# Kernel tuning notes

Measured on AMD Instinct MI355X. Metric: run time of the kernel, lower is better.

The kernel has to match this reference:

```python
import jax, jax.numpy as jnp
import numpy as np


def _gru_dir(x, Wih, Whh, bih, bhh):
    # x: (B,T,I) -> (B,T,H); torch GRU equations, h0 = 0
    H = Whh.shape[1]
    pre = x @ Wih.T + bih  # (B,T,3H), input projection hoisted out of scan
    def step(h, p):
        gh = h @ Whh.T + bhh
        pr, pz, pn = jnp.split(p, 3, axis=-1)
        gr, gz, gn = jnp.split(gh, 3, axis=-1)
        r = jax.nn.sigmoid(pr + gr)
        z = jax.nn.sigmoid(pz + gz)
        n = jnp.tanh(pn + r * gn)
        h = (1.0 - z) * n + z * h
        return h, h
    h0 = jnp.zeros((x.shape[0], H), x.dtype)
    _, ys = jax.lax.scan(step, h0, jnp.swapaxes(pre, 0, 1))
    return jnp.swapaxes(ys, 0, 1)


def _gru_bidir(x, Wih, Whh, bih, bhh):
    f = _gru_dir(x, Wih[0], Whh[0], bih[0], bhh[0])
    b = _gru_dir(x[:, ::-1], Wih[1], Whh[1], bih[1], bhh[1])[:, ::-1]
    return jnp.concatenate([f, b], axis=-1)


def _forward(inputs, embed, l_Wih, l_Whh, l_bih, l_bhh, r_Wih, r_Whh, r_bih, r_bhh,
             a_Wih, a_Whh, a_bih, a_bhh, Wc1, Wc2, vc, Wb, Wd, vd, Wm, vm, Ws, vs,
             Wp, vp, Wpred):
    x = embed[inputs]  # (B,T,E)
    hl = _gru_bidir(x, l_Wih, l_Whh, l_bih, l_bhh)  # (B,T,2H)
    hr = _gru_bidir(x, r_Wih, r_Whh, r_bih, r_bhh)  # (B,T,2H)
    # co-attention: score[b,i,j] = vc . tanh(Wc1 hl_j + Wc2 hr_i)
    s = jnp.tanh((hl @ Wc1.T)[:, None, :, :] + (hr @ Wc2.T)[:, :, None, :])  # (B,T,T,H)
    ptc = jax.nn.softmax((s @ vc.T)[..., 0], axis=-1) @ hl
    # bilinear: hr (Wb hl)^T
    sjt = jnp.einsum('bid,bjd->bij', hr, hl @ Wb.T)
    ptb = jax.nn.softmax(sjt, axis=-1) @ hl
    # multiplicative: vd . tanh(Wd (hl_j * hr_i))
    p = hl[:, None, :, :] * hr[:, :, None, :]  # (B,T,T,2H)
    ptd = jax.nn.softmax((jnp.tanh(p @ Wd.T) @ vd.T)[..., 0], axis=-1) @ hl
    # subtractive: vm . tanh(Wm (hl_j - hr_i))
    d = hl[:, None, :, :] - hr[:, :, None, :]  # (B,T,T,2H)
    ptm = jax.nn.softmax((jnp.tanh(d @ Wm.T) @ vm.T)[..., 0], axis=-1) @ hl
    # self-attention on hr: vs . tanh(Ws (hr_j * hr_i))
    ss = hr[:, None, :, :] * hr[:, :, None, :]  # (B,T,T,2H)
    pts = jax.nn.softmax((jnp.tanh(ss @ Ws.T) @ vs.T)[..., 0], axis=-1) @ hr
    agg = jnp.concatenate([hr, pts, ptc, ptd, ptb, ptm], axis=-1)  # (B,T,12H)
    ar = _gru_bidir(agg, a_Wih, a_Whh, a_bih, a_bhh)  # (B,T,2H)
    # pooling of hl
    sj = jax.nn.softmax(jnp.swapaxes(jnp.tanh(hl @ Wp.T) @ vp.T, 1, 2), axis=-1)  # (B,1,T)
    rl = sj @ hl  # (B,1,2H)
    # final attention over aggregation
    sj2 = jax.nn.softmax(jnp.swapaxes((ar @ Wc1.T + rl @ Wc2.T) @ vc.T, 1, 2), axis=-1)  # (B,1,T)
    rr = (sj2 @ ar)[:, 0, :]  # (B,2H)
    return jax.nn.sigmoid(rr @ Wpred.T)  # (B,labels)


def setup_inputs() -> dict:
    B, T, V, E, H, L = 4, 256, 30000, 300, 128, 2
    key = jax.random.key(0)
    ks = jax.random.split(key, 40)
    inp = {}
    inp['inputs'] = jax.random.randint(ks[0], (B, T), 0, V)
    inp['embed'] = jax.random.uniform(ks[1], (V, E), jnp.float32, -0.1, 0.1)
    ki = 2
    for name, isz in [('l', E), ('r', E), ('a', 12 * H)]:
        inp[name + '_Wih'] = jax.random.normal(ks[ki], (2, 3 * H, isz), jnp.float32) * 0.05; ki += 1
        inp[name + '_Whh'] = jax.random.normal(ks[ki], (2, 3 * H, H), jnp.float32) * 0.05; ki += 1
        inp[name + '_bih'] = jnp.zeros((2, 3 * H), jnp.float32)
        inp[name + '_bhh'] = jnp.zeros((2, 3 * H), jnp.float32)
    for n, o, i in [('Wc1', H, 2 * H), ('Wc2', H, 2 * H), ('vc', 1, H), ('Wb', 2 * H, 2 * H),
                    ('Wd', H, 2 * H), ('vd', 1, H), ('Wm', H, 2 * H), ('vm', 1, H),
                    ('Ws', H, 2 * H), ('vs', 1, H), ('Wp', H, 2 * H), ('vp', 1, H),
                    ('Wpred', L, 2 * H)]:
        inp[n] = jax.random.normal(ks[ki], (o, i), jnp.float32) * 0.05; ki += 1
    return inp


def reference(inputs, embed, l_Wih, l_Whh, l_bih, l_bhh, r_Wih, r_Whh, r_bih, r_bhh,
              a_Wih, a_Whh, a_bih, a_bhh, Wc1, Wc2, vc, Wb, Wd, vd, Wm, vm, Ws, vs,
              Wp, vp, Wpred):
    return _forward(inputs, embed, l_Wih, l_Whh, l_bih, l_bhh, r_Wih, r_Whh, r_bih,
                    r_bhh, a_Wih, a_Whh, a_bih, a_bhh, Wc1, Wc2, vc, Wb, Wd, vd, Wm,
                    vm, Ws, vs, Wp, vp, Wpred)
```

## Files before the change

kernel.cpp:

```cpp
#include <hip/hip_runtime.h>


#define DEV static __device__ __forceinline__
#define BAR_LGKM() __asm__ volatile("s_waitcnt lgkmcnt(0)\ns_barrier" ::: "memory")

typedef __attribute__((ext_vector_type(4))) float f32x4;
typedef __attribute__((ext_vector_type(8))) short s16x8;
typedef __attribute__((ext_vector_type(4))) unsigned int u32x4;
typedef __attribute__((ext_vector_type(2))) unsigned int u32x2;

constexpr int T = 256, E = 300, EP = 320, H = 128, H2 = 256, H3 = 384, H12 = 1536;
constexpr int M = 1024;
constexpr int STY = 262144;

DEV float b2f(unsigned short h) { return __uint_as_float(((unsigned)h) << 16); }
DEV unsigned short f2b(float f) {
  unsigned u = __float_as_uint(f);
  u += 0x7fff + ((u >> 16) & 1);
  return (unsigned short)(u >> 16);
}
DEV unsigned cvt_pk_bf16(float lo, float hi) {
  unsigned r;
  __asm__("v_cvt_pk_bf16_f32 %0, %1, %2" : "=v"(r) : "v"(lo), "v"(hi));
  return r;
}
DEV float rcp_f(float x) {
  float r;
  __asm__("v_rcp_f32 %0, %1" : "=v"(r) : "v"(x));
  return r;
}
DEV float sigm(float x) { return rcp_f(1.f + __expf(-x)); }
DEV float tanh_f(float x) {
  float e = __expf(2.f * x);
  return __builtin_fmaf(-2.f, rcp_f(e + 1.f), 1.f);
}
DEV float plsel(float x0, float x1) {
  u32x2 r = __builtin_amdgcn_permlane32_swap(
      __float_as_uint(x0), __float_as_uint(x1), false, false);
  return __uint_as_float(r[0]);
}

DEV s16x8 ldfrag(const unsigned short* p) {
  u32x4 v = *(const u32x4*)p;
  return __builtin_bit_cast(s16x8, v);
}
DEV f32x4 mfma16(s16x8 a, s16x8 b, f32x4 c) {
  return __builtin_amdgcn_mfma_f32_16x16x32_bf16(a, b, c, 0, 0, 0);
}


struct StageArgs {
  const float* cs[3]; unsigned short* cd[3]; int cn[3];
  const int* idx; const float* emb; unsigned short* xhi; unsigned short* xlo;
  const float* lW; const float* rW; unsigned short* wpad;
  int bo[6];
};

__global__ void k_stage(StageArgs sa) {
  int blk = blockIdx.x;
  int seg = 0;
  #pragma unroll
  for (int s2 = 1; s2 < 5; ++s2) seg = (blk >= sa.bo[s2]) ? s2 : seg;
  int i = (blk - sa.bo[seg]) * 256 + threadIdx.x;
  if (seg < 3) {
    if (i < sa.cn[seg]) sa.cd[seg][i] = f2b(sa.cs[seg][i]);
    return;
  }
  if (seg == 3) {
    if (i >= M * EP) return;
    int m = i / EP, e = i - m * EP;
    int r = sa.idx[m];
    float v = (e < E) ? sa.emb[(size_t)r * E + e] : 0.f;
    unsigned short hi = f2b(v);
    sa.xhi[i] = hi;
    sa.xlo[i] = f2b(v - b2f(hi));
    return;
  }
  if (i >= 4 * H3 * EP) return;
  int e = i % EP, n = (i / EP) % H3, uu = i / (EP * H3);
  const float* src = (uu < 2 ? sa.lW : sa.rW) + (size_t)((uu & 1) * H3 + n) * E;
  sa.wpad[i] = (e < E) ? f2b(src[e]) : (unsigned short)0;
}


struct GemmDesc {
  const unsigned short* Ahi; const unsigned short* Alo; const unsigned short* W;
  const float* bias; float* Cf; int N; int K; int tr;
};
struct GemmBatch { GemmDesc d[8]; };

DEV void gemm_body(const GemmDesc& g, int mb, int nb, int tid) {
  int lane = tid & 63, w = tid >> 6, quad = lane >> 4, l16 = lane & 15;
  int K = g.K;
  const unsigned short* Ahp = g.Ahi + (size_t)(mb + w * 16 + l16) * K + quad * 8;
  const unsigned short* Alp = g.Alo + (size_t)(mb + w * 16 + l16) * K + quad * 8;
  const unsigned short* Wp = g.W + (size_t)(nb + l16) * K + quad * 8;
  f32x4 acc[4];
  #pragma unroll
  for (int nt = 0; nt < 4; ++nt) acc[nt] = f32x4{0.f, 0.f, 0.f, 0.f};
  for (int k = 0; k < K; k += 32) {
    s16x8 ah = ldfrag(Ahp + k);
    s16x8 al = ldfrag(Alp + k);
    #pragma unroll
    for (int nt = 0; nt < 4; ++nt) {
      s16x8 b = ldfrag(Wp + (size_t)nt * 16 * K + k);
      acc[nt] = mfma16(ah, b, acc[nt]);
      acc[nt] = mfma16(al, b, acc[nt]);
    }
  }
  int mr0 = mb + w * 16 + quad * 4;
  #pragma unroll
  for (int nt = 0; nt < 4; ++nt) {
    int col = nb + nt * 16 + l16;
    float bv = g.bias ? g.bias[col] : 0.f;
    #pragma unroll
    for (int r = 0; r < 4; ++r) {
      if (g.tr)
        g.Cf[(size_t)col * M + (mr0 + r)] = acc[nt][r] + bv;
      else
        g.Cf[(size_t)(mr0 + r) * g.N + col] = acc[nt][r] + bv;
    }
  }
}

__global__ __launch_bounds__(256) void k_gemm(GemmBatch gb) {
  GemmDesc g = gb.d[blockIdx.z];
  int nb = blockIdx.y * 64;
  if (nb >= g.N) return;
  gemm_body(g, blockIdx.x * 64, nb, threadIdx.x);
}


struct RecArgs {
  const unsigned short* whh[4];
  const float* pre[4];
  float* outf[4];
  unsigned short* outhi[4];
  unsigned short* outlo[4];
  unsigned short* agghi[4];
  unsigned short* agglo[4];
  const float* bhh[4];
  int colOff[4];
  int dir[4];
  int nGru;
  const float* ccs[6]; unsigned short* ccd[6]; int ccn[6]; int cbo[7];
  const float *Hp, *hlf, *vpf, *Wc2f; float* rlcl;
  const float* Wc1f; const float* vcf; float* uOut;
};

#define GRU_STEP(pr_, pz_, pn_, pq_, hcur_, hnxt_)                             \
  {                                                                            \
    float pr = pr_, pz = pz_, pn = pn_;                                        \
    pq_ += pst2;                                                               \
    pr_ = pq_[0] + bh_r; pz_ = pq_[128] + bh_z; pn_ = pq_[256];                \
    const unsigned short* hb_ = hcur_ + l16 * 136 + quad * 8;                  \
    s16x8 ah0 = ldfrag(hb_);                                                   \
    s16x8 ah1 = ldfrag(hb_ + 32);                                              \
    s16x8 ah2 = ldfrag(hb_ + 64);                                              \
    s16x8 ah3 = ldfrag(hb_ + 96);                                              \
    f32x4 z4 = f32x4{0.f, 0.f, 0.f, 0.f};                                      \
    f32x4 aR0 = mfma16(ah0, bq[0][0], z4);                                     \
    f32x4 aR1 = mfma16(ah2, bq[0][2], z4);                                     \
    aR0 = mfma16(ah1, bq[0][1], aR0);                                          \
    aR1 = mfma16(ah3, bq[0][3], aR1);                                          \
    f32x4 aZ0 = mfma16(ah0, bq[1][0], z4);                                     \
    f32x4 aZ1 = mfma16(ah2, bq[1][2], z4);                                     \
    aZ0 = mfma16(ah1, bq[1][1], aZ0);                                          \
    aZ1 = mfma16(ah3, bq[1][3], aZ1);                                          \
    float r0 = (aR0[0] + aR1[0]) + (aR0[1] + aR1[1]);                          \
    float r1v = (aR0[2] + aR1[2]) + (aR0[3] + aR1[3]);                         \
    float rg = sigm(pr + plsel(r0, r1v));                                      \
    f32x4 aN0 = mfma16(ah0, bq[2][0], z4);                                     \
    f32x4 aN1 = mfma16(ah2, bq[2][2], z4);                                     \
    aN0 = mfma16(ah1, bq[2][1], aN0);                                          \
    aN1 = mfma16(ah3, bq[2][3], aN1);                                          \
    float z0 = (aZ0[0] + aZ1[0]) + (aZ0[1] + aZ1[1]);                          \
    float z1 = (aZ0[2] + aZ1[2]) + (aZ0[3] + aZ1[3]);                          \
    float zg = sigm(pz + plsel(z0, z1));                                       \
    float n0 = (aN0[0] + aN1[0]) + (aN0[1] + aN1[1]);                          \
    float n1 = (aN0[2] + aN1[2]) + (aN0[3] + aN1[3]);                          \
    float ng = tanh_f(pn + rg * (plsel(n0, n1) + bh_n));                       \
    hf = __builtin_fmaf(zg, hf - ng, ng);                                      \
    unsigned hp32 = cvt_pk_bf16(hf, hf);                                       \
    float rem = hf - __uint_as_float(hp32 << 16);                              \
    unsigned lp32 = cvt_pk_bf16(rem, rem);                                     \
    unsigned short hi = (unsigned short)hp32;                                  \
    unsigned short lo = (unsigned short)lp32;                                  \
    hnxt_[(2 * b) * 136 + d] = hi;                                             \
    hnxt_[(2 * b + 1) * 136 + d] = lo;                                         \
    *outf_p = hf; *outhi_p = hi; *outlo_p = lo;                                \
    outf_p += ost; outhi_p += ost; outlo_p += ost;                             \
    if (agghi_p) { *agghi_p = hi; *agglo_p = lo; agghi_p += ast; agglo_p += ast; } \
    BAR_LGKM();                                                                \
  }

__global__ __launch_bounds__(512) void k_gru(RecArgs ra) {
  int blk = blockIdx.x;
  int tid = threadIdx.x;
  if (blk >= ra.nGru) {
    if (ra.rlcl) {
      int b = blk - ra.nGru;
      if (b >= 4) {
        if (tid < 256) {
          float acc = 0.f;
          for (int h = 0; h < 128; ++h)
            acc += ra.vcf[h] * ra.Wc1f[(size_t)h * 256 + tid];
          ra.uOut[tid] = acc;
        }
        return;
      }
      __shared__ float vl[128], wl[256], rvec[256], red[4];
      if (tid < 128) vl[tid] = ra.vpf[tid];
      __syncthreads();
      float s = 0.f, e = 0.f;
      if (tid < 256) {
        const float* hp = ra.Hp + (size_t)(b * 256 + tid) * 128;
        for (int k = 0; k < 128; ++k) s += vl[k] * tanh_f(hp[k]);
        float m = s;
        for (int dl = 32; dl; dl >>= 1) m = fmaxf(m, __shfl_xor(m, dl));
        if ((tid & 63) == 0) red[tid >> 6] = m;
      }
      __syncthreads();
      float m = fmaxf(fmaxf(red[0], red[1]), fmaxf(red[2], red[3]));
      __syncthreads();
      if (tid < 256) {
        e = __expf(s - m);
        float sum = e;
        for (int dl = 32; dl; dl >>= 1) sum += __shfl_xor(sum, dl);
        if ((tid & 63) == 0) red[tid >> 6] = sum;
      }
      __syncthreads();
      float sum = red[0] + red[1] + red[2] + red[3];
      if (tid < 256) wl[tid] = e * rcp_f(sum);
      __syncthreads();
      if (tid < 256) {
        float acc = 0.f;
        for (int t = 0; t < 256; ++t)
          acc += wl[t] * ra.hlf[(size_t)(b * 256 + t) * 256 + tid];
        rvec[tid] = acc;
      }
      __syncthreads();
      if (tid < 128) {
        float a2 = 0.f;
        const float* wr = ra.Wc2f + (size_t)tid * 256;
        for (int dk = 0; dk < 256; ++dk) a2 += rvec[dk] * wr[dk];
        ra.rlcl[b * 128 + tid] = a2;
      }
      return;
    }
    int cb = blk - ra.nGru;
    int seg = 0;
    #pragma unroll
    for (int s2 = 1; s2 < 6; ++s2) seg = (cb >= ra.cbo[s2]) ? s2 : seg;
    int i = (cb - ra.cbo[seg]) * 512 + tid;
    if (i < ra.ccn[seg]) ra.ccd[seg][i] = f2b(ra.ccs[seg][i]);
    return;
  }
  int u = blk;
  __shared__ __align__(16) unsigned short hs[2][16 * 136];
  int lane = tid & 63, w8 = tid >> 6;
  int quad = lane >> 4, l16 = lane & 15;
  for (int i = tid; i < 2 * 16 * 136; i += 512) ((unsigned short*)hs)[i] = 0;
  const unsigned short* whh = ra.whh[u];
  s16x8 bq[3][4];
  #pragma unroll
  for (int g = 0; g < 3; ++g) {
    int row = g * 128 + w8 * 16 + l16;
    #pragma unroll
    for (int kc = 0; kc < 4; ++kc)
      bq[g][kc] = ldfrag(whh + (size_t)row * H + kc * 32 + quad * 8);
  }
  const float* bhh = ra.bhh[u];
  const float* pre = ra.pre[u];
  int colOff = ra.colOff[u], dir = ra.dir[u];
  int b = ((quad & 1) << 1) | (quad >> 1);
  int d = w8 * 16 + l16;
  float bh_r = bhh[d], bh_z = bhh[d + 128], bh_n = bhh[d + 256];
  float hf = 0.f;
  int t0 = dir ? (T - 1) : 0;
  long pst = dir ? -(long)H3 : (long)H3;
  long pst2 = 2 * pst;
  long ost = dir ? -(long)H2 : (long)H2;
  long ast = dir ? -(long)H12 : (long)H12;
  size_t o0 = (size_t)(b * T + t0) * H2 + colOff + d;
  size_t a0 = (size_t)(b * T + t0) * H12 + colOff + d;
  float* outf_p = ra.outf[u] + o0;
  unsigned short* outhi_p = ra.outhi[u] + o0;
  unsigned short* outlo_p = ra.outlo[u] + o0;
  unsigned short* agghi_p = ra.agghi[u] ? ra.agghi[u] + a0 : nullptr;
  unsigned short* agglo_p = ra.agglo[u] ? ra.agglo[u] + a0 : nullptr;
  const float* pqE = pre + (size_t)(b * T + t0) * H3 + d;
  const float* pqO = pqE + pst;
  float e_pr = pqE[0] + bh_r, e_pz = pqE[128] + bh_z, e_pn = pqE[256];
  float o_pr = pqO[0] + bh_r, o_pz = pqO[128] + bh_z, o_pn = pqO[256];
  __syncthreads();
  for (int s = 0; s < T; s += 2) {
    GRU_STEP(e_pr, e_pz, e_pn, pqE, hs[0], hs[1]);
    GRU_STEP(o_pr, o_pz, o_pn, pqO, hs[1], hs[0]);
  }
}


struct ScMMArgs {
  const unsigned short* Xhi[2];
  const float* Rf; const float* Wt[2]; const float* vt[2];
  float* So[2];
};
struct FuseArgs { GemmDesc d[6]; ScMMArgs sm; };

__global__ __launch_bounds__(512, 2) void k_fuse(FuseArgs fa) {
  __shared__ __align__(16) unsigned short w_lds[128 * 256];
  int y = blockIdx.y;
  int tid = threadIdx.x;
  if (y < 6) {
    int xx = blockIdx.x;
    if (xx >= 32) return;
    GemmDesc g = fa.d[y];
    int nb = (xx >> 3) * 64;
    if (nb >= g.N) return;
    int mb = (xx & 7) * 128 + (tid >> 8) * 64;
    gemm_body(g, mb, nb, tid & 255);
    return;
  }
  const ScMMArgs& a = fa.sm;
  int type = y - 6;
  int bi = blockIdx.x, b = bi >> 8;
  const unsigned short* Xhi = a.Xhi[type];
  const float* W = a.Wt[type];
  const float* v = a.vt[type];
  float* Sout = a.So[type];
  int lane = tid & 63, w = tid >> 6, quad = lane >> 4, l16 = lane & 15;
  int d4 = tid & 63, rhi = tid >> 6;
  float4 h4 = ((const float4*)(a.Rf + (size_t)bi * 256))[d4];
  #pragma unroll
  for (int it = 0; it < 16; ++it) {
    int kl = it * 8 + rhi;
    float4 w4 = ((const float4*)(W + (size_t)kl * 256))[d4];
    unsigned lo32 = cvt_pk_bf16(w4.x * h4.x, w4.y * h4.y);
    unsigned hi32 = cvt_pk_bf16(w4.z * h4.z, w4.w * h4.w);
    unsigned long long pk = (unsigned long long)lo32 | ((unsigned long long)hi32 << 32);
    int gphys = ((d4 >> 1) + kl) & 31;
    *(unsigned long long*)(w_lds + (size_t)kl * 256 + gphys * 8 + (d4 & 1) * 4) = pk;
  }
  BAR_LGKM();
  f32x4 acc[2][8];
  #pragma unroll
  for (int jj = 0; jj < 2; ++jj)
    #pragma unroll
    for (int c = 0; c < 8; ++c) acc[jj][c] = f32x4{0.f, 0.f, 0.f, 0.f};
  const unsigned short* Xp0 =
      Xhi + (size_t)(b * 256 + w * 2 * 16 + l16) * 256 + quad * 8;
  #pragma unroll 2
  for (int kc = 0; kc < 8; ++kc) {
    s16x8 bf0 = ldfrag(Xp0 + kc * 32);
    s16x8 bf1 = ldfrag(Xp0 + (size_t)16 * 256 + kc * 32);
    #pragma unroll
    for (int c = 0; c < 8; ++c) {
      int krow = c * 16 + l16;
      int gp = (kc * 4 + quad + krow) & 31;
      s16x8 af = ldfrag(w_lds + (size_t)krow * 256 + gp * 8);
      acc[0][c] = mfma16(af, bf0, acc[0][c]);
      acc[1][c] = mfma16(af, bf1, acc[1][c]);
    }
  }
  #pragma unroll
  for (int jj = 0; jj < 2; ++jj) {
    float s = 0.f;
    #pragma unroll
    for (int c = 0; c < 8; ++c)
      #pragma unroll
      for (int r = 0; r < 4; ++r)
        s += tanh_f(acc[jj][c][r]) * v[c * 16 + quad * 4 + r];
    s += __shfl_xor(s, 16);
    s += __shfl_xor(s, 32);
    int jt = w * 2 + jj;
    if (lane < 16) Sout[(size_t)bi * 256 + jt * 16 + l16] = s;
  }
}


struct ScCmbArgs {
  const float *Hc, *Rc, *Hm, *Rm, *HB, *hrf, *vcf, *vmf; float* S;
  const float* hlf;
  unsigned short *ahi, *alo;
};

__global__ __launch_bounds__(256, 2) void k_sccmb(ScCmbArgs a) {
  int bi = blockIdx.x;
  int tid = threadIdx.x;
  if (bi >= 256) {
    int widx = bi - 256;
    int type = (widx >> 7) * 2;
    int rem = widx & 127;
    int it = rem >> 2, b = rem & 3;
    __shared__ float p_l[8][256];
    __shared__ float red[4];
    for (int ii = 0; ii < 8; ++ii) {
      size_t idx = ((size_t)(b * 256 + it * 8 + ii)) * 256 + tid;
      float x = a.S[(size_t)type * STY + idx];
      float m = x;
      for (int dl = 32; dl; dl >>= 1) m = fmaxf(m, __shfl_xor(m, dl));
      if ((tid & 63) == 0) red[tid >> 6] = m;
      __syncthreads();
      m = fmaxf(fmaxf(red[0], red[1]), fmaxf(red[2], red[3]));
      __syncthreads();
      float e = __expf(x - m);
      float sum = e;
      for (int dl = 32; dl; dl >>= 1) sum += __shfl_xor(sum, dl);
      if ((tid & 63) == 0) red[tid >> 6] = sum;
      __syncthreads();
      sum = red[0] + red[1] + red[2] + red[3];
      p_l[ii][tid] = e * rcp_f(sum);
      __syncthreads();
    }
    const float* src = (type == 0 ? a.hrf : a.hlf) + (size_t)b * 256 * 256;
    float acc[8] = {0.f, 0.f, 0.f, 0.f, 0.f, 0.f, 0.f, 0.f};
    for (int j = 0; j < 256; ++j) {
      float hv = src[(size_t)j * 256 + tid];
      #pragma unroll
      for (int ii = 0; ii < 8; ++ii) acc[ii] += p_l[ii][j] * hv;
    }
    int off = 256 * (1 + type);
    #pragma unroll
    for (int ii = 0; ii < 8; ++ii) {
      float vv = acc[ii];
      unsigned short hi = f2b(vv);
      size_t o = (size_t)(b * 256 + it * 8 + ii) * H12 + off + tid;
      a.ahi[o] = hi;
      a.alo[o] = f2b(vv - b2f(hi));
    }
    return;
  }
  __shared__ float rc_l[4 * 128];
  __shared__ float rm_l[4 * 128];
  __shared__ float hr_l[4 * 256];
  __shared__ float vc_l[128], vm_l[128];
  int b = bi >> 6, i0 = (bi & 63) << 2;
  int gi0 = b * 256 + i0;
  {
    const float4* hr4 = (const float4*)(a.hrf + (size_t)gi0 * 256);
    ((float4*)hr_l)[tid] = hr4[tid];
    if (tid < 128) {
      const float4* rc4 = (const float4*)(a.Rc + (size_t)gi0 * 128);
      const float4* rm4 = (const float4*)(a.Rm + (size_t)gi0 * 128);
      ((float4*)rc_l)[tid] = rc4[tid];
      ((float4*)rm_l)[tid] = rm4[tid];
      vc_l[tid] = a.vcf[tid]; vm_l[tid] = a.vmf[tid];
    }
  }
  __syncthreads();
  int j = tid;
  size_t cb = (size_t)(b * 256 + j);
  float scq[4], smq[4], sbq[4];
  #pragma unroll
  for (int q = 0; q < 4; ++q) { scq[q] = 0.f; smq[q] = 0.f; sbq[q] = 0.f; }
  for (int k = 0; k < 128; ++k) {
    float hc = a.Hc[(size_t)k * M + cb];
    float hm = a.Hm[(size_t)k * M + cb];
    float vck = vc_l[k], vmk = vm_l[k];
    #pragma unroll
    for (int q = 0; q < 4; ++q) {
      scq[q] += vck * tanh_f(hc + rc_l[q * 128 + k]);
      smq[q] += vmk * tanh_f(hm - rm_l[q * 128 + k]);
    }
  }
  for (int k = 0; k < 256; ++k) {
    float hb = a.HB[(size_t)k * M + cb];
    #pragma unroll
    for (int q = 0; q < 4; ++q) sbq[q] += hb * hr_l[q * 256 + k];
  }
  #pragma unroll
  for (int q = 0; q < 4; ++q) {
    size_t o = (size_t)(gi0 + q) * 256 + j;
    a.S[(size_t)STY * 1 + o] = scq[q];
    a.S[(size_t)STY * 3 + o] = sbq[q];
    a.S[(size_t)STY * 4 + o] = smq[q];
  }
}


__global__ __launch_bounds__(256) void k_wsum(const float* __restrict__ S,
    const float* __restrict__ hl_f, const float* __restrict__ hr_f,
    unsigned short* __restrict__ ahi, unsigned short* __restrict__ alo) {
  int it = blockIdx.x, b = blockIdx.z;
  int y = blockIdx.y;
  int type = (y == 0) ? 1 : (y + 2);
  __shared__ float p_l[8][256];
  __shared__ float red[4];
  int tid = threadIdx.x;
  for (int ii = 0; ii < 8; ++ii) {
    size_t idx = ((size_t)(b * 256 + it * 8 + ii)) * 256 + tid;
    float x = S[(size_t)type * STY + idx];
    float m = x;
    for (int dl = 32; dl; dl >>= 1) m = fmaxf(m, __shfl_xor(m, dl));
    if ((tid & 63) == 0) red[tid >> 6] = m;
    __syncthreads();
    m = fmaxf(fmaxf(red[0], red[1]), fmaxf(red[2], red[3]));
    __syncthreads();
    float e = __expf(x - m);
    float sum = e;
    for (int dl = 32; dl; dl >>= 1) sum += __shfl_xor(sum, dl);
    if ((tid & 63) == 0) red[tid >> 6] = sum;
    __syncthreads();
    sum = red[0] + red[1] + red[2] + red[3];
    p_l[ii][tid] = e * rcp_f(sum);
    __syncthreads();
  }
  const float* src = hl_f + (size_t)b * 256 * 256;
  float acc[8] = {0.f, 0.f, 0.f, 0.f, 0.f, 0.f, 0.f, 0.f};
  for (int j = 0; j < 256; ++j) {
    float hv = src[(size_t)j * 256 + tid];
    #pragma unroll
    for (int ii = 0; ii < 8; ++ii) acc[ii] += p_l[ii][j] * hv;
  }
  int off = 256 * (1 + type);
  #pragma unroll
  for (int ii = 0; ii < 8; ++ii) {
    float vv = acc[ii];
    unsigned short hi = f2b(vv);
    size_t o = (size_t)(b * 256 + it * 8 + ii) * H12 + off + tid;
    ahi[o] = hi;
    alo[o] = f2b(vv - b2f(hi));
  }
}


__global__ __launch_bounds__(256) void k_tail(const float* __restrict__ u,
    const float* __restrict__ rlcl, const float* __restrict__ ar_f,
    const float* __restrict__ vcf, const float* __restrict__ Wpredf,
    float* __restrict__ out) {
  int b = blockIdx.x, tid = threadIdx.x;
  __shared__ float ul[256], wl[256], rvec[256], red[4], vc_l[128], rl_l[128];
  ul[tid] = u[tid];
  if (tid < 128) { vc_l[tid] = vcf[tid]; rl_l[tid] = rlcl[b * 128 + tid]; }
  __syncthreads();
  float c0 = 0.f;
  for (int h = 0; h < 128; ++h) c0 += vc_l[h] * rl_l[h];
  const float* ar = ar_f + (size_t)(b * 256 + tid) * 256;
  float s2 = c0;
  for (int k = 0; k < 256; ++k) s2 += ul[k] * ar[k];
  float m = s2;
  for (int dl = 32; dl; dl >>= 1) m = fmaxf(m, __shfl_xor(m, dl));
  if ((tid & 63) == 0) red[tid >> 6] = m;
  __syncthreads();
  m = fmaxf(fmaxf(red[0], red[1]), fmaxf(red[2], red[3]));
  __syncthreads();
  float e2 = __expf(s2 - m);
  float sum2 = e2;
  for (int dl = 32; dl; dl >>= 1) sum2 += __shfl_xor(sum2, dl);
  if ((tid & 63) == 0) red[tid >> 6] = sum2;
  __syncthreads();
  sum2 = red[0] + red[1] + red[2] + red[3];
  wl[tid] = e2 * rcp_f(sum2);
  __syncthreads();
  float acc2 = 0.f;
  for (int t = 0; t < 256; ++t) acc2 += wl[t] * ar_f[(size_t)(b * 256 + t) * 256 + tid];
  rvec[tid] = acc2;
  __syncthreads();
  if (tid < 2) {
    float o = 0.f;
    const float* wp = Wpredf + (size_t)tid * 256;
    for (int dk = 0; dk < 256; ++dk) o += rvec[dk] * wp[dk];
    out[b * 2 + tid] = sigm(o);
  }
}


extern "C" void kernel_launch(void* const* d_in, const int* in_sizes, int n_in,
                              void* d_out, int out_size, void* d_ws, size_t ws_size,
                              hipStream_t stream) {
  (void)in_sizes; (void)n_in; (void)out_size; (void)ws_size;
  const int* inputs = (const int*)d_in[0];
  const float* embed = (const float*)d_in[1];
  const float* lWih = (const float*)d_in[2];
  const float* lWhh = (const float*)d_in[3];
  const float* lbih = (const float*)d_in[4];
  const float* lbhh = (const float*)d_in[5];
  const float* rWih = (const float*)d_in[6];
  const float* rWhh = (const float*)d_in[7];
  const float* rbih = (const float*)d_in[8];
  const float* rbhh = (const float*)d_in[9];
  const float* aWih = (const float*)d_in[10];
  const float* aWhh = (const float*)d_in[11];
  const float* abih = (const float*)d_in[12];
  const float* abhh = (const float*)d_in[13];
  const float* Wc1 = (const float*)d_in[14];
  const float* Wc2 = (const float*)d_in[15];
  const float* vc  = (const float*)d_in[16];
  const float* Wb  = (const float*)d_in[17];
  const float* Wd  = (const float*)d_in[18];
  const float* vd  = (const float*)d_in[19];
  const float* Wm  = (const float*)d_in[20];
  const float* vmv = (const float*)d_in[21];
  const float* Wsw = (const float*)d_in[22];
  const float* vsv = (const float*)d_in[23];
  const float* Wp  = (const float*)d_in[24];
  const float* vp  = (const float*)d_in[25];
  const float* Wpred = (const float*)d_in[26];

  char* ws = (char*)d_ws;
  size_t off = 0;
  auto alloc = [&](size_t bytes) -> void* {
    void* p = ws + off;
    off += (bytes + 255) & ~(size_t)255;
    return p;
  };
  unsigned short* xhi = (unsigned short*)alloc((size_t)M * EP * 2);
  unsigned short* xlo = (unsigned short*)alloc((size_t)M * EP * 2);
  unsigned short* wpad = (unsigned short*)alloc((size_t)4 * H3 * EP * 2);
  unsigned short* Whh_b = (unsigned short*)alloc((size_t)6 * H3 * H * 2);
  unsigned short* aWih_b = (unsigned short*)alloc((size_t)2 * H3 * H12 * 2);
  unsigned short* Wc1_b = (unsigned short*)alloc((size_t)H * H2 * 2);
  unsigned short* Wc2_b = (unsigned short*)alloc((size_t)H * H2 * 2);
  unsigned short* Wm_b  = (unsigned short*)alloc((size_t)H * H2 * 2);
  unsigned short* Wp_b  = (unsigned short*)alloc((size_t)H * H2 * 2);
  unsigned short* Wb_b  = (unsigned short*)alloc((size_t)H2 * H2 * 2);
  char* region1 = (char*)alloc((size_t)4 * M * H3 * 4);
  float* pre_lr = (float*)region1;
  float* S      = (float*)region1;
  float* pre_a  = (float*)region1;
  float* hl_f = (float*)alloc((size_t)M * H2 * 4);
  float* hr_f = (float*)alloc((size_t)M * H2 * 4);
  unsigned short* hl_hi = (unsigned short*)alloc((size_t)M * H2 * 2);
  unsigned short* hl_lo = (unsigned short*)alloc((size_t)M * H2 * 2);
  unsigned short* hr_hi = (unsigned short*)alloc((size_t)M * H2 * 2);
  unsigned short* hr_lo = (unsigned short*)alloc((size_t)M * H2 * 2);
  float* Hc = (float*)alloc((size_t)M * H * 4);
  float* Rc = (float*)alloc((size_t)M * H * 4);
  float* Hm = (float*)alloc((size_t)M * H * 4);
  float* Rm = (float*)alloc((size_t)M * H * 4);
  float* Hp = (float*)alloc((size_t)M * H * 4);
  float* HB = (float*)alloc((size_t)M * H2 * 4);
  unsigned short* agg_hi = (unsigned short*)alloc((size_t)M * H12 * 2);
  unsigned short* agg_lo = (unsigned short*)alloc((size_t)M * H12 * 2);
  float* ar_f = (float*)alloc((size_t)M * H2 * 4);
  unsigned short* ar_hi = (unsigned short*)alloc((size_t)M * H2 * 2);
  unsigned short* ar_lo = (unsigned short*)alloc((size_t)M * H2 * 2);
  float* rlcl = (float*)alloc((size_t)4 * H * 4);
  float* ubuf = (float*)alloc((size_t)H2 * 4);

  StageArgs sa{};
  sa.cs[0] = lWhh;  sa.cd[0] = Whh_b;                 sa.cn[0] = 2 * H3 * H;
  sa.cs[1] = rWhh;  sa.cd[1] = Whh_b + 2 * H3 * H;    sa.cn[1] = 2 * H3 * H;
  sa.cs[2] = aWhh;  sa.cd[2] = Whh_b + 4 * H3 * H;    sa.cn[2] = 2 * H3 * H;
  sa.idx = inputs; sa.emb = embed; sa.xhi = xhi; sa.xlo = xlo;
  sa.lW = lWih; sa.rW = rWih; sa.wpad = wpad;
  {
    int acc0 = 0;
    sa.bo[0] = 0;
    for (int s = 0; s < 3; ++s) { acc0 += (sa.cn[s] + 255) / 256; sa.bo[s + 1] = acc0; }
    acc0 += (M * EP + 255) / 256;       sa.bo[4] = acc0;
    acc0 += (4 * H3 * EP + 255) / 256;  sa.bo[5] = acc0;
  }
  k_stage<<<dim3(sa.bo[5]), dim3(256), 0, stream>>>(sa);

  GemmBatch ga{};
  const float* biases[4] = { lbih, lbih + H3, rbih, rbih + H3 };
  for (int u = 0; u < 4; ++u)
    ga.d[u] = GemmDesc{ xhi, xlo, wpad + (size_t)u * H3 * EP, biases[u],
                        pre_lr + (size_t)u * M * H3, H3, EP, 0 };
  k_gemm<<<dim3(16, 6, 4), dim3(256), 0, stream>>>(ga);

  RecArgs r1{};
  r1.whh[0] = Whh_b;               r1.whh[1] = Whh_b + H3 * H;
  r1.whh[2] = Whh_b + 2 * H3 * H;  r1.whh[3] = Whh_b + 3 * H3 * H;
  for (int u = 0; u < 4; ++u) r1.pre[u] = pre_lr + (size_t)u * M * H3;
  r1.outf[0] = r1.outf[1] = hl_f; r1.outf[2] = r1.outf[3] = hr_f;
  r1.outhi[0] = r1.outhi[1] = hl_hi; r1.outhi[2] = r1.outhi[3] = hr_hi;
  r1.outlo[0] = r1.outlo[1] = hl_lo; r1.outlo[2] = r1.outlo[3] = hr_lo;
  r1.agghi[0] = r1.agghi[1] = nullptr; r1.agghi[2] = r1.agghi[3] = agg_hi;
  r1.agglo[0] = r1.agglo[1] = nullptr; r1.agglo[2] = r1.agglo[3] = agg_lo;
  r1.bhh[0] = lbhh; r1.bhh[1] = lbhh + H3; r1.bhh[2] = rbhh; r1.bhh[3] = rbhh + H3;
  r1.colOff[0] = 0; r1.colOff[1] = H; r1.colOff[2] = 0; r1.colOff[3] = H;
  r1.dir[0] = 0; r1.dir[1] = 1; r1.dir[2] = 0; r1.dir[3] = 1;
  r1.nGru = 4;
  r1.ccs[0] = aWih; r1.ccd[0] = aWih_b; r1.ccn[0] = 2 * H3 * H12;
  r1.ccs[1] = Wc1;  r1.ccd[1] = Wc1_b;  r1.ccn[1] = H * H2;
  r1.ccs[2] = Wc2;  r1.ccd[2] = Wc2_b;  r1.ccn[2] = H * H2;
  r1.ccs[3] = Wm;   r1.ccd[3] = Wm_b;   r1.ccn[3] = H * H2;
  r1.ccs[4] = Wp;   r1.ccd[4] = Wp_b;   r1.ccn[4] = H * H2;
  r1.ccs[5] = Wb;   r1.ccd[5] = Wb_b;   r1.ccn[5] = H2 * H2;
  int cvtBlocks;
  {
    int acc0 = 0;
    r1.cbo[0] = 0;
    for (int s = 0; s < 6; ++s) { acc0 += (r1.ccn[s] + 511) / 512; r1.cbo[s + 1] = acc0; }
    cvtBlocks = acc0;
  }
  r1.Hp = nullptr; r1.hlf = nullptr; r1.vpf = nullptr; r1.Wc2f = nullptr;
  r1.rlcl = nullptr; r1.Wc1f = nullptr; r1.vcf = nullptr; r1.uOut = nullptr;
  k_gru<<<dim3(4 + cvtBlocks), dim3(512), 0, stream>>>(r1);

  FuseArgs fu{};
  fu.d[0] = GemmDesc{ hl_hi, hl_lo, Wc1_b, nullptr, Hc, H, H2, 1 };
  fu.d[1] = GemmDesc{ hr_hi, hr_lo, Wc2_b, nullptr, Rc, H, H2, 0 };
  fu.d[2] = GemmDesc{ hl_hi, hl_lo, Wm_b, nullptr, Hm, H, H2, 1 };
  fu.d[3] = GemmDesc{ hr_hi, hr_lo, Wm_b, nullptr, Rm, H, H2, 0 };
  fu.d[4] = GemmDesc{ hl_hi, hl_lo, Wb_b, nullptr, HB, H2, H2, 1 };
  fu.d[5] = GemmDesc{ hl_hi, hl_lo, Wp_b, nullptr, Hp, H, H2, 0 };
  fu.sm.Xhi[0] = hl_hi; fu.sm.Wt[0] = Wd;  fu.sm.vt[0] = vd;
  fu.sm.So[0] = S + (size_t)2 * STY;
  fu.sm.Xhi[1] = hr_hi; fu.sm.Wt[1] = Wsw; fu.sm.vt[1] = vsv;
  fu.sm.So[1] = S + (size_t)0 * STY;
  fu.sm.Rf = hr_f;
  k_fuse<<<dim3(M, 8), dim3(512), 0, stream>>>(fu);

  ScCmbArgs scb{};
  scb.Hc = Hc; scb.Rc = Rc; scb.Hm = Hm; scb.Rm = Rm; scb.HB = HB;
  scb.hrf = hr_f; scb.vcf = vc; scb.vmf = vmv; scb.S = S;
  scb.hlf = hl_f; scb.ahi = agg_hi; scb.alo = agg_lo;
  k_sccmb<<<dim3(512), dim3(256), 0, stream>>>(scb);

  k_wsum<<<dim3(32, 3, 4), dim3(256), 0, stream>>>(S, hl_f, hr_f, agg_hi, agg_lo);

  GemmBatch gc{};
  gc.d[0] = GemmDesc{ agg_hi, agg_lo, aWih_b, abih, pre_a, H3, H12, 0 };
  gc.d[1] = GemmDesc{ agg_hi, agg_lo, aWih_b + (size_t)H3 * H12, abih + H3,
                      pre_a + (size_t)M * H3, H3, H12, 0 };
  k_gemm<<<dim3(16, 6, 2), dim3(256), 0, stream>>>(gc);

  RecArgs r2{};
  r2.whh[0] = Whh_b + 4 * H3 * H; r2.whh[1] = Whh_b + 5 * H3 * H;
  r2.whh[2] = r2.whh[3] = Whh_b + 4 * H3 * H;
  r2.pre[0] = pre_a; r2.pre[1] = pre_a + (size_t)M * H3;
  r2.pre[2] = r2.pre[3] = pre_a;
  r2.outf[0] = r2.outf[1] = r2.outf[2] = r2.outf[3] = ar_f;
  r2.outhi[0] = r2.outhi[1] = r2.outhi[2] = r2.outhi[3] = ar_hi;
  r2.outlo[0] = r2.outlo[1] = r2.outlo[2] = r2.outlo[3] = ar_lo;
  for (int u = 0; u < 4; ++u) { r2.agghi[u] = nullptr; r2.agglo[u] = nullptr; }
  r2.bhh[0] = abhh; r2.bhh[1] = abhh + H3; r2.bhh[2] = r2.bhh[3] = abhh;
  r2.colOff[0] = 0; r2.colOff[1] = H; r2.colOff[2] = r2.colOff[3] = 0;
  r2.dir[0] = 0; r2.dir[1] = 1; r2.dir[2] = r2.dir[3] = 0;
  r2.nGru = 2;
  for (int s = 0; s < 6; ++s) { r2.ccs[s] = nullptr; r2.ccd[s] = nullptr; r2.ccn[s] = 0; }
  for (int s = 0; s < 7; ++s) r2.cbo[s] = 0;
  r2.Hp = Hp; r2.hlf = hl_f; r2.vpf = vp; r2.Wc2f = Wc2; r2.rlcl = rlcl;
  r2.Wc1f = Wc1; r2.vcf = vc; r2.uOut = ubuf;
  k_gru<<<dim3(2 + 5), dim3(512), 0, stream>>>(r2);

  k_tail<<<dim3(4), dim3(256), 0, stream>>>(ubuf, rlcl, ar_f, vc, Wpred,
                                            (float*)d_out);
}
```

Measured before the change: 616.5 us.

## Split aggregation-GRU input GEMM by K and overlap slices with producer kernels

Splits the agg @ a_Wih projection along K by which agg column segments are ready. K 0-255 (hr) runs inside k_fuse, K 256-511 and 768-1023 (pts, ptd) run as extra blocks in k_wsum, and the rest runs in a smaller final k_gemm that accumulates into pre_a. pre_a gets its own buffer, so the extra blocks no longer alias the S region. This hides part of the large GEMM behind the attention kernels. In exchange it adds read-modify-write accumulation passes over pre_a and relies on kernel ordering for the accumulate writes to be correct.

New measurement: 613.3 us. About the same (-0.5%).

```diff
diff --git a/kernel.cpp b/kernel.cpp
--- a/kernel.cpp
+++ b/kernel.cpp
@@ -85,25 +85,24 @@
 
 struct GemmDesc {
   const unsigned short* Ahi; const unsigned short* Alo; const unsigned short* W;
-  const float* bias; float* Cf; int N; int K; int tr;
+  const float* bias; float* Cf; int N; int K; int lda; int ldw; int tr; int accum;
 };
 struct GemmBatch { GemmDesc d[8]; };
 
 DEV void gemm_body(const GemmDesc& g, int mb, int nb, int tid) {
   int lane = tid & 63, w = tid >> 6, quad = lane >> 4, l16 = lane & 15;
-  int K = g.K;
-  const unsigned short* Ahp = g.Ahi + (size_t)(mb + w * 16 + l16) * K + quad * 8;
-  const unsigned short* Alp = g.Alo + (size_t)(mb + w * 16 + l16) * K + quad * 8;
-  const unsigned short* Wp = g.W + (size_t)(nb + l16) * K + quad * 8;
+  const unsigned short* Ahp = g.Ahi + (size_t)(mb + w * 16 + l16) * g.lda + quad * 8;
+  const unsigned short* Alp = g.Alo + (size_t)(mb + w * 16 + l16) * g.lda + quad * 8;
+  const unsigned short* Wp = g.W + (size_t)(nb + l16) * g.ldw + quad * 8;
   f32x4 acc[4];
   #pragma unroll
   for (int nt = 0; nt < 4; ++nt) acc[nt] = f32x4{0.f, 0.f, 0.f, 0.f};
-  for (int k = 0; k < K; k += 32) {
+  for (int k = 0; k < g.K; k += 32) {
     s16x8 ah = ldfrag(Ahp + k);
     s16x8 al = ldfrag(Alp + k);
     #pragma unroll
     for (int nt = 0; nt < 4; ++nt) {
-      s16x8 b = ldfrag(Wp + (size_t)nt * 16 * K + k);
+      s16x8 b = ldfrag(Wp + (size_t)nt * 16 * g.ldw + k);
       acc[nt] = mfma16(ah, b, acc[nt]);
       acc[nt] = mfma16(al, b, acc[nt]);
     }
@@ -112,13 +111,19 @@
   #pragma unroll
   for (int nt = 0; nt < 4; ++nt) {
     int col = nb + nt * 16 + l16;
-    float bv = g.bias ? g.bias[col] : 0.f;
-    #pragma unroll
-    for (int r = 0; r < 4; ++r) {
-      if (g.tr)
-        g.Cf[(size_t)col * M + (mr0 + r)] = acc[nt][r] + bv;
-      else
-        g.Cf[(size_t)(mr0 + r) * g.N + col] = acc[nt][r] + bv;
+    if (g.accum) {
+      #pragma unroll
+      for (int r = 0; r < 4; ++r)
+        g.Cf[(size_t)(mr0 + r) * g.N + col] += acc[nt][r];
+    } else {
+      float bv = g.bias ? g.bias[col] : 0.f;
+      #pragma unroll
+      for (int r = 0; r < 4; ++r) {
+        if (g.tr)
+          g.Cf[(size_t)col * M + (mr0 + r)] = acc[nt][r] + bv;
+        else
+          g.Cf[(size_t)(mr0 + r) * g.N + col] = acc[nt][r] + bv;
+      }
     }
   }
 }
@@ -306,7 +311,7 @@
   const float* Rf; const float* Wt[2]; const float* vt[2];
   float* So[2];
 };
-struct FuseArgs { GemmDesc d[6]; ScMMArgs sm; };
+struct FuseArgs { GemmDesc d[8]; ScMMArgs sm; };
 
 __global__ __launch_bounds__(512, 2) void k_fuse(FuseArgs fa) {
   __shared__ __align__(16) unsigned short w_lds[128 * 256];
@@ -318,6 +323,15 @@
     GemmDesc g = fa.d[y];
     int nb = (xx >> 3) * 64;
     if (nb >= g.N) return;
+    int mb = (xx & 7) * 128 + (tid >> 8) * 64;
+    gemm_body(g, mb, nb, tid & 255);
+    return;
+  }
+  if (y >= 8) {
+    int xx = blockIdx.x;
+    if (xx >= 48) return;
+    GemmDesc g = fa.d[y - 2];
+    int nb = (xx >> 3) * 64;
     int mb = (xx & 7) * 128 + (tid >> 8) * 64;
     gemm_body(g, mb, nb, tid & 255);
     return;
@@ -481,13 +495,29 @@
 
 __global__ __launch_bounds__(256) void k_wsum(const float* __restrict__ S,
     const float* __restrict__ hl_f, const float* __restrict__ hr_f,
-    unsigned short* __restrict__ ahi, unsigned short* __restrict__ alo) {
+    unsigned short* __restrict__ ahi, unsigned short* __restrict__ alo,
+    const unsigned short* __restrict__ aW, float* __restrict__ preA) {
+  int tid = threadIdx.x;
+  if (blockIdx.y == 3) {
+    int t3 = (blockIdx.z * 32 + blockIdx.x) * 3;
+    for (int q = 0; q < 3; ++q) {
+      int t = t3 + q;
+      if (t >= 384) break;
+      int unit = t / 192, rem = t % 192, seg = rem / 96, rem2 = rem % 96;
+      int mtile = rem2 / 6, ntile = rem2 % 6;
+      int k0 = seg ? 768 : 256;
+      GemmDesc g{ ahi + k0, alo + k0,
+                  aW + (size_t)unit * H3 * H12 + k0, nullptr,
+                  preA + (size_t)unit * M * H3, H3, 256, H12, H12, 0, 1 };
+      gemm_body(g, mtile * 64, ntile * 64, tid);
+    }
+    return;
+  }
   int it = blockIdx.x, b = blockIdx.z;
   int y = blockIdx.y;
   int type = (y == 0) ? 1 : (y + 2);
   __shared__ float p_l[8][256];
   __shared__ float red[4];
-  int tid = threadIdx.x;
   for (int ii = 0; ii < 8; ++ii) {
     size_t idx = ((size_t)(b * 256 + it * 8 + ii)) * 256 + tid;
     float x = S[(size_t)type * STY + idx];
@@ -618,7 +648,7 @@
   char* region1 = (char*)alloc((size_t)4 * M * H3 * 4);
   float* pre_lr = (float*)region1;
   float* S      = (float*)region1;
-  float* pre_a  = (float*)region1;
+  float* pre_a  = (float*)alloc((size_t)2 * M * H3 * 4);
   float* hl_f = (float*)alloc((size_t)M * H2 * 4);
   float* hr_f = (float*)alloc((size_t)M * H2 * 4);
   unsigned short* hl_hi = (unsigned short*)alloc((size_t)M * H2 * 2);
@@ -658,7 +688,7 @@
   const float* biases[4] = { lbih, lbih + H3, rbih, rbih + H3 };
   for (int u = 0; u < 4; ++u)
     ga.d[u] = GemmDesc{ xhi, xlo, wpad + (size_t)u * H3 * EP, biases[u],
-                        pre_lr + (size_t)u * M * H3, H3, EP, 0 };
+                        pre_lr + (size_t)u * M * H3, H3, EP, EP, EP, 0, 0 };
   k_gemm<<<dim3(16, 6, 4), dim3(256), 0, stream>>>(ga);
 
   RecArgs r1{};
@@ -692,18 +722,22 @@
   k_gru<<<dim3(4 + cvtBlocks), dim3(512), 0, stream>>>(r1);
 
   FuseArgs fu{};
-  fu.d[0] = GemmDesc{ hl_hi, hl_lo, Wc1_b, nullptr, Hc, H, H2, 1 };
-  fu.d[1] = GemmDesc{ hr_hi, hr_lo, Wc2_b, nullptr, Rc, H, H2, 0 };
-  fu.d[2] = GemmDesc{ hl_hi, hl_lo, Wm_b, nullptr, Hm, H, H2, 1 };
-  fu.d[3] = GemmDesc{ hr_hi, hr_lo, Wm_b, nullptr, Rm, H, H2, 0 };
-  fu.d[4] = GemmDesc{ hl_hi, hl_lo, Wb_b, nullptr, HB, H2, H2, 1 };
-  fu.d[5] = GemmDesc{ hl_hi, hl_lo, Wp_b, nullptr, Hp, H, H2, 0 };
+  fu.d[0] = GemmDesc{ hl_hi, hl_lo, Wc1_b, nullptr, Hc, H, H2, H2, H2, 1, 0 };
+  fu.d[1] = GemmDesc{ hr_hi, hr_lo, Wc2_b, nullptr, Rc, H, H2, H2, H2, 0, 0 };
+  fu.d[2] = GemmDesc{ hl_hi, hl_lo, Wm_b, nullptr, Hm, H, H2, H2, H2, 1, 0 };
+  fu.d[3] = GemmDesc{ hr_hi, hr_lo, Wm_b, nullptr, Rm, H, H2, H2, H2, 0, 0 };
+  fu.d[4] = GemmDesc{ hl_hi, hl_lo, Wb_b, nullptr, HB, H2, H2, H2, H2, 1, 0 };
+  fu.d[5] = GemmDesc{ hl_hi, hl_lo, Wp_b, nullptr, Hp, H, H2, H2, H2, 0, 0 };
+  fu.d[6] = GemmDesc{ agg_hi, agg_lo, aWih_b, abih, pre_a,
+                      H3, 256, H12, H12, 0, 0 };
+  fu.d[7] = GemmDesc{ agg_hi, agg_lo, aWih_b + (size_t)H3 * H12, abih + H3,
+                      pre_a + (size_t)M * H3, H3, 256, H12, H12, 0, 0 };
   fu.sm.Xhi[0] = hl_hi; fu.sm.Wt[0] = Wd;  fu.sm.vt[0] = vd;
   fu.sm.So[0] = S + (size_t)2 * STY;
   fu.sm.Xhi[1] = hr_hi; fu.sm.Wt[1] = Wsw; fu.sm.vt[1] = vsv;
   fu.sm.So[1] = S + (size_t)0 * STY;
   fu.sm.Rf = hr_f;
-  k_fuse<<<dim3(M, 8), dim3(512), 0, stream>>>(fu);
+  k_fuse<<<dim3(M, 10), dim3(512), 0, stream>>>(fu);
 
   ScCmbArgs scb{};
   scb.Hc = Hc; scb.Rc = Rc; scb.Hm = Hm; scb.Rm = Rm; scb.HB = HB;
@@ -711,13 +745,19 @@
   scb.hlf = hl_f; scb.ahi = agg_hi; scb.alo = agg_lo;
   k_sccmb<<<dim3(512), dim3(256), 0, stream>>>(scb);
 
-  k_wsum<<<dim3(32, 3, 4), dim3(256), 0, stream>>>(S, hl_f, hr_f, agg_hi, agg_lo);
+  k_wsum<<<dim3(32, 4, 4), dim3(256), 0, stream>>>(S, hl_f, hr_f, agg_hi, agg_lo,
+                                                   aWih_b, pre_a);
 
   GemmBatch gc{};
-  gc.d[0] = GemmDesc{ agg_hi, agg_lo, aWih_b, abih, pre_a, H3, H12, 0 };
-  gc.d[1] = GemmDesc{ agg_hi, agg_lo, aWih_b + (size_t)H3 * H12, abih + H3,
-                      pre_a + (size_t)M * H3, H3, H12, 0 };
-  k_gemm<<<dim3(16, 6, 2), dim3(256), 0, stream>>>(gc);
+  for (int u = 0; u < 2; ++u) {
+    gc.d[2 * u + 0] = GemmDesc{ agg_hi + 512, agg_lo + 512,
+                                aWih_b + (size_t)u * H3 * H12 + 512, nullptr,
+                                pre_a + (size_t)u * M * H3, H3, 256, H12, H12, 0, 1 };
+    gc.d[2 * u + 1] = GemmDesc{ agg_hi + 1024, agg_lo + 1024,
+                                aWih_b + (size_t)u * H3 * H12 + 1024, nullptr,
+                                pre_a + (size_t)u * M * H3, H3, 512, H12, H12, 0, 1 };
+  }
+  k_gemm<<<dim3(16, 6, 4), dim3(256), 0, stream>>>(gc);
 
   RecArgs r2{};
   r2.whh[0] = Whh_b + 4 * H3 * H; r2.whh[1] = Whh_b + 5 * H3 * H;
```
